# Optimization experiments

Hardware: AMD Instinct MI355X
Metric: run time of the kernel (lower is better)

Reference implementation:

```python
import jax, jax.numpy as jnp
import numpy as np

K = 64        # top-k from init_kwargs
TAU = 1.0     # temperature at step=0: tau_start*(1-0) + tau_end*0


def setup_inputs() -> dict:
    key = jax.random.key(0)
    k1, k2 = jax.random.split(key)
    B, N = 2048, 8192
    logits = jax.random.normal(k1, (B, N), dtype=jnp.float32)
    # gumbels = -log(Exp(1)) == standard Gumbel noise
    gumbel_noise = jax.random.gumbel(k2, (B, N), dtype=jnp.float32)
    return {"logits": logits, "gumbel_noise": gumbel_noise}


def reference(logits, gumbel_noise):
    # training path of GumbelTopK (step=0 -> tau=TAU, hard=True)
    g = (logits + gumbel_noise) / TAU                       # [B, N]
    order = jnp.argsort(-g, axis=-1)                        # descending sort order
    sorted_g = jnp.take_along_axis(g, order, axis=-1)
    cumsum = jnp.cumsum(jax.nn.softmax(sorted_g, axis=-1), axis=-1)
    mask = (cumsum <= K).astype(sorted_g.dtype)             # NB: faithful to source (<= k)
    sorted_y = mask * jax.nn.softmax(sorted_g / TAU, axis=-1)
    # scatter back to original positions == gather by inverse permutation
    inv = jnp.argsort(order, axis=-1)
    y = jnp.take_along_axis(sorted_y, inv, axis=-1)         # [B, N]
    # hard straight-through: one-hot-k of y
    k = min(K, y.shape[-1])
    _, idx = jax.lax.top_k(y, k)                            # [B, k]
    rows = jnp.arange(y.shape[0])[:, None]
    y_hard = jnp.zeros_like(y).at[rows, idx].set(1.0)
    return jax.lax.stop_gradient(y_hard - y) + y
```

## Files before the change

kernel.cpp:

```cpp
#include <hip/hip_runtime.h>

constexpr int N = 8192;
constexpr int K = 64;
constexpr int THREADS = 256;
constexpr int WAVES = THREADS / 64;
constexpr int EPT = N / THREADS;
constexpr int VEC = EPT / 4;
constexpr int SEGCAP = 64;
constexpr int CAP = 1024;

constexpr float FTHRESH = 4.75f;

typedef float f32x4 __attribute__((ext_vector_type(4)));

__device__ __forceinline__ unsigned orderable(float f) {
    unsigned x = __float_as_uint(f);
    return (x & 0x80000000u) ? ~x : (x | 0x80000000u);
}

__device__ __forceinline__ void barrier_nd() {
    asm volatile("s_waitcnt lgkmcnt(0)" ::: "memory");
    __builtin_amdgcn_s_barrier();
    asm volatile("" ::: "memory");
}

__global__ __launch_bounds__(THREADS, 8)
void gumbel_topk_onehot(const float* __restrict__ logits,
                        const float* __restrict__ noise,
                        float* __restrict__ out)
{
    __shared__ __align__(16) unsigned hist[2048];
    __shared__ __align__(16) unsigned cand[CAP];
    __shared__ __align__(16) unsigned seg[WAVES][SEGCAP];
    __shared__ unsigned scnt[WAVES];
    __shared__ unsigned wavesum[WAVES];
    __shared__ unsigned ccount;
    __shared__ unsigned sel_bin, sel_kth, sel_cnt;
    __shared__ unsigned r_val, r_take, r_ceq;

    const int tid  = threadIdx.x;
    const int lane = tid & 63;
    const int wave = tid >> 6;
    const long long row = blockIdx.x;

    const f32x4* l4 = (const f32x4*)(logits + row * (long long)N);
    const f32x4* n4 = (const f32x4*)(noise  + row * (long long)N);
    float s[EPT];
#pragma unroll
    for (int g4 = 0; g4 < VEC; g4 += 2) {
        f32x4 a0 = l4[tid + (g4 + 0) * THREADS];
        f32x4 a1 = l4[tid + (g4 + 1) * THREADS];
        f32x4 b0 = n4[tid + (g4 + 0) * THREADS];
        f32x4 b1 = n4[tid + (g4 + 1) * THREADS];
#pragma unroll
        for (int e = 0; e < 4; ++e) s[4 * g4 + e]     = a0[e] + b0[e];
#pragma unroll
        for (int e = 0; e < 4; ++e) s[4 * g4 + 4 + e] = a1[e] + b1[e];
    }

    const unsigned long long below = (1ull << lane) - 1ull;
    unsigned cw = 0;
#pragma unroll
    for (int e = 0; e < EPT; ++e) {
        const bool p = (s[e] >= FTHRESH);
        const unsigned long long m = __ballot(p);
        if (p) {
            const unsigned pos = cw + (unsigned)__popcll(m & below);
            if (pos < (unsigned)SEGCAP) seg[wave][pos] = __float_as_uint(s[e]);
        }
        cw += (unsigned)__popcll(m);
    }
    if (lane == 0) scnt[wave] = cw;
    barrier_nd();

    const unsigned c0 = scnt[0], c1 = scnt[1], c2 = scnt[2], c3 = scnt[3];
    const unsigned c  = c0 + c1 + c2 + c3;
    const unsigned mx = max(max(c0, c1), max(c2, c3));
    const unsigned cws[WAVES] = {c0, c1, c2, c3};

    float Tf;
    unsigned take_eq, c_eq;
    bool fast;

    if (c >= (unsigned)K && c <= (unsigned)THREADS && mx <= (unsigned)SEGCAP) {
        const bool have = (tid < (int)c);
        unsigned myv = 0u;
        if (have) {
            unsigned d = (unsigned)tid, w2 = 0;
            if (d >= c0) { d -= c0; w2 = 1;
                if (d >= c1) { d -= c1; w2 = 2;
                    if (d >= c2) { d -= c2; w2 = 3; } } }
            myv = seg[w2][d];
        }
        if (tid < (int)((c + 63u) & ~63u)) {
            unsigned g = 0, eq = 0;
#pragma unroll
            for (int w2 = 0; w2 < WAVES; ++w2) {
                const unsigned cn = cws[w2];
                const uint4* s4 = (const uint4*)seg[w2];
                for (unsigned q = 0; q * 4 < cn; ++q) {
                    const uint4 v = s4[q];
                    const unsigned i0 = q * 4;
                    if (i0 + 0 < cn) { g += v.x > myv; eq += v.x == myv; }
                    if (i0 + 1 < cn) { g += v.y > myv; eq += v.y == myv; }
                    if (i0 + 2 < cn) { g += v.z > myv; eq += v.z == myv; }
                    if (i0 + 3 < cn) { g += v.w > myv; eq += v.w == myv; }
                }
            }
            if (have && g < (unsigned)K && g + eq >= (unsigned)K) {
                r_val  = myv;
                r_take = (unsigned)K - g;
                r_ceq  = eq;
            }
        }
        barrier_nd();
        Tf      = __uint_as_float(r_val);
        take_eq = r_take;
        c_eq    = r_ceq;
        fast    = (take_eq == c_eq);
    } else {
        unsigned kth = K;

#define SELECT_BIN(BPT)                                                      \
        {                                                                    \
            unsigned p = 0;                                                  \
            _Pragma("unroll")                                                \
            for (int j = 0; j < (BPT); ++j) p += hist[tid * (BPT) + j];      \
            unsigned sc = p;                                                 \
            _Pragma("unroll")                                                \
            for (int off = 1; off < 64; off <<= 1) {                         \
                unsigned v = __shfl_down(sc, off);                           \
                if (lane + off < 64) sc += v;                                \
            }                                                                \
            if (lane == 0) wavesum[wave] = sc;                               \
            __syncthreads();                                                 \
            unsigned S = sc;                                                 \
            _Pragma("unroll")                                                \
            for (int w = 0; w < WAVES; ++w) if (w > wave) S += wavesum[w];   \
            unsigned Snext = S - p;                                          \
            if (S >= kth && Snext < kth) {                                   \
                unsigned cum = Snext;                                        \
                for (int j = (BPT) - 1; j >= 0; --j) {                       \
                    unsigned b = tid * (BPT) + j;                            \
                    unsigned cc = hist[b];                                   \
                    if (cum + cc >= kth) {                                   \
                        sel_bin = b;                                         \
                        sel_kth = kth - cum;                                 \
                        sel_cnt = cc;                                        \
                        break;                                               \
                    }                                                        \
                    cum += cc;                                               \
                }                                                            \
            }                                                                \
            __syncthreads();                                                 \
        }

        for (int i = tid; i < 512; i += THREADS)
            ((uint4*)hist)[i] = make_uint4(0u, 0u, 0u, 0u);
        if (tid == 0) ccount = 0u;
        __syncthreads();
#pragma unroll
        for (int e = 0; e < EPT; ++e)
            atomicAdd(&hist[orderable(s[e]) >> 21], 1u);
        __syncthreads();
        SELECT_BIN(8)
        const unsigned b1   = sel_bin;
        const unsigned cnt1 = sel_cnt;
        kth = sel_kth;

#pragma unroll
        for (int e = 0; e < EPT; ++e) {
            const unsigned k_e = orderable(s[e]);
            if ((k_e >> 21) == b1) {
                const unsigned pos = atomicAdd(&ccount, 1u);
                if (pos < (unsigned)CAP) cand[pos] = k_e & 0x1FFFFFu;
            }
        }
        __syncthreads();
        const bool use_cand = (cnt1 <= (unsigned)CAP);

        for (int i = tid; i < 512; i += THREADS)
            ((uint4*)hist)[i] = make_uint4(0u, 0u, 0u, 0u);
        __syncthreads();
        if (use_cand) {
            for (int i = tid; i < (int)cnt1; i += THREADS)
                atomicAdd(&hist[cand[i] >> 10], 1u);
        } else {
#pragma unroll
            for (int e = 0; e < EPT; ++e) {
                const unsigned k_e = orderable(s[e]);
                if ((k_e >> 21) == b1)
                    atomicAdd(&hist[(k_e >> 10) & 0x7FFu], 1u);
            }
        }
        __syncthreads();
        SELECT_BIN(8)
        const unsigned b2 = sel_bin;
        kth = sel_kth;
        __syncthreads();

        for (int i = tid; i < 256; i += THREADS)
            ((uint4*)hist)[i] = make_uint4(0u, 0u, 0u, 0u);
        __syncthreads();
        if (use_cand) {
            for (int i = tid; i < (int)cnt1; i += THREADS) {
                const unsigned cv = cand[i];
                if ((cv >> 10) == b2) atomicAdd(&hist[cv & 0x3FFu], 1u);
            }
        } else {
            const unsigned pfx = (b1 << 11) | b2;
#pragma unroll
            for (int e = 0; e < EPT; ++e) {
                const unsigned k_e = orderable(s[e]);
                if ((k_e >> 10) == pfx)
                    atomicAdd(&hist[k_e & 0x3FFu], 1u);
            }
        }
        __syncthreads();
        SELECT_BIN(4)
        const unsigned T_ord = (b1 << 21) | (b2 << 10) | sel_bin;
        const unsigned bits = (T_ord & 0x80000000u) ? (T_ord & 0x7FFFFFFFu)
                                                    : ~T_ord;
        Tf      = __uint_as_float(bits);
        take_eq = sel_kth;
        c_eq    = sel_cnt;
        fast    = (take_eq == c_eq);
#undef SELECT_BIN
    }

    f32x4* orow = (f32x4*)(out + row * (long long)N);
    if (fast) {
#pragma unroll
        for (int i = 0; i < VEC; ++i) {
            f32x4 o;
            o.x = (s[4*i+0] >= Tf) ? 1.0f : 0.0f;
            o.y = (s[4*i+1] >= Tf) ? 1.0f : 0.0f;
            o.z = (s[4*i+2] >= Tf) ? 1.0f : 0.0f;
            o.w = (s[4*i+3] >= Tf) ? 1.0f : 0.0f;
            orow[tid + i * THREADS] = o;
        }
    } else {
#pragma unroll
        for (int i = 0; i < VEC; ++i) {
            f32x4 o;
            o.x = (s[4*i+0] > Tf) ? 1.0f : 0.0f;
            o.y = (s[4*i+1] > Tf) ? 1.0f : 0.0f;
            o.z = (s[4*i+2] > Tf) ? 1.0f : 0.0f;
            o.w = (s[4*i+3] > Tf) ? 1.0f : 0.0f;
            orow[tid + i * THREADS] = o;
        }
        __syncthreads();
        if (tid == 0) {
            const float* lf = logits + row * (long long)N;
            const float* nf = noise  + row * (long long)N;
            float* of = out + row * (long long)N;
            unsigned cc = 0;
            for (int i = 0; i < N; ++i) {
                if (lf[i] + nf[i] == Tf) {
                    of[i] = 1.0f;
                    if (++cc == take_eq) break;
                }
            }
        }
    }
}

extern "C" void kernel_launch(void* const* d_in, const int* in_sizes, int n_in,
                              void* d_out, int out_size, void* d_ws, size_t ws_size,
                              hipStream_t stream) {
    const float* logits = (const float*)d_in[0];
    const float* noise  = (const float*)d_in[1];
    float* out = (float*)d_out;
    const int rows = in_sizes[0] / N;
    gumbel_topk_onehot<<<rows, THREADS, 0, stream>>>(logits, noise, out);
}
```

Baseline: 190.4 us.

## Stream row without register cache, zero-fill output, scatter top-k ones by index

```diff
diff --git a/kernel.cpp b/kernel.cpp
--- a/kernel.cpp
+++ b/kernel.cpp
@@ -4,10 +4,8 @@
 constexpr int K = 64;
 constexpr int THREADS = 256;
 constexpr int WAVES = THREADS / 64;
-constexpr int EPT = N / THREADS;
-constexpr int VEC = EPT / 4;
+constexpr int F4PT = (N / 4) / THREADS;
 constexpr int SEGCAP = 64;
-constexpr int CAP = 1024;
 
 constexpr float FTHRESH = 4.75f;
 
@@ -30,13 +28,13 @@
                         float* __restrict__ out)
 {
     __shared__ __align__(16) unsigned hist[2048];
-    __shared__ __align__(16) unsigned cand[CAP];
-    __shared__ __align__(16) unsigned seg[WAVES][SEGCAP];
+    __shared__ __align__(16) float    segv[WAVES][SEGCAP];
+    __shared__ __align__(16) unsigned segi[WAVES][SEGCAP];
     __shared__ unsigned scnt[WAVES];
     __shared__ unsigned wavesum[WAVES];
-    __shared__ unsigned ccount;
     __shared__ unsigned sel_bin, sel_kth, sel_cnt;
-    __shared__ unsigned r_val, r_take, r_ceq;
+    __shared__ float    sh_T;
+    __shared__ unsigned sh_take, sh_ceq;
 
     const int tid  = threadIdx.x;
     const int lane = tid & 63;
@@ -45,30 +43,39 @@
 
     const f32x4* l4 = (const f32x4*)(logits + row * (long long)N);
     const f32x4* n4 = (const f32x4*)(noise  + row * (long long)N);
-    float s[EPT];
-#pragma unroll
-    for (int g4 = 0; g4 < VEC; g4 += 2) {
-        f32x4 a0 = l4[tid + (g4 + 0) * THREADS];
-        f32x4 a1 = l4[tid + (g4 + 1) * THREADS];
-        f32x4 b0 = n4[tid + (g4 + 0) * THREADS];
-        f32x4 b1 = n4[tid + (g4 + 1) * THREADS];
-#pragma unroll
-        for (int e = 0; e < 4; ++e) s[4 * g4 + e]     = a0[e] + b0[e];
-#pragma unroll
-        for (int e = 0; e < 4; ++e) s[4 * g4 + 4 + e] = a1[e] + b1[e];
-    }
+    f32x4*       o4 = (f32x4*)(out + row * (long long)N);
+    float*     orow = out + row * (long long)N;
 
     const unsigned long long below = (1ull << lane) - 1ull;
+    const f32x4 zero4 = {0.f, 0.f, 0.f, 0.f};
+
     unsigned cw = 0;
 #pragma unroll
-    for (int e = 0; e < EPT; ++e) {
-        const bool p = (s[e] >= FTHRESH);
-        const unsigned long long m = __ballot(p);
-        if (p) {
-            const unsigned pos = cw + (unsigned)__popcll(m & below);
-            if (pos < (unsigned)SEGCAP) seg[wave][pos] = __float_as_uint(s[e]);
-        }
-        cw += (unsigned)__popcll(m);
+    for (int g = 0; g < F4PT; g += 2) {
+        f32x4 a0 = l4[tid + (g + 0) * THREADS];
+        f32x4 a1 = l4[tid + (g + 1) * THREADS];
+        f32x4 b0 = n4[tid + (g + 0) * THREADS];
+        f32x4 b1 = n4[tid + (g + 1) * THREADS];
+        o4[tid + (g + 0) * THREADS] = zero4;
+        o4[tid + (g + 1) * THREADS] = zero4;
+        float sv[8];
+#pragma unroll
+        for (int e = 0; e < 4; ++e) { sv[e] = a0[e] + b0[e]; sv[4 + e] = a1[e] + b1[e]; }
+        const unsigned i0 = 4u * (unsigned)(tid + (g + 0) * THREADS);
+        const unsigned i1 = 4u * (unsigned)(tid + (g + 1) * THREADS);
+#pragma unroll
+        for (int e = 0; e < 8; ++e) {
+            const bool p = (sv[e] >= FTHRESH);
+            const unsigned long long m = __ballot(p);
+            if (p) {
+                const unsigned pos = cw + (unsigned)__popcll(m & below);
+                if (pos < (unsigned)SEGCAP) {
+                    segv[wave][pos] = sv[e];
+                    segi[wave][pos] = (e < 4) ? (i0 + e) : (i1 + e - 4);
+                }
+            }
+            cw += (unsigned)__popcll(m);
+        }
     }
     if (lane == 0) scnt[wave] = cw;
     barrier_nd();
@@ -76,48 +83,59 @@
     const unsigned c0 = scnt[0], c1 = scnt[1], c2 = scnt[2], c3 = scnt[3];
     const unsigned c  = c0 + c1 + c2 + c3;
     const unsigned mx = max(max(c0, c1), max(c2, c3));
-    const unsigned cws[WAVES] = {c0, c1, c2, c3};
-
-    float Tf;
-    unsigned take_eq, c_eq;
-    bool fast;
-
-    if (c >= (unsigned)K && c <= (unsigned)THREADS && mx <= (unsigned)SEGCAP) {
-        const bool have = (tid < (int)c);
-        unsigned myv = 0u;
+
+    if (c >= (unsigned)K && mx <= (unsigned)SEGCAP) {
+        const unsigned cws[WAVES] = {c0, c1, c2, c3};
+        const bool have = ((unsigned)tid < c);
+        float myv = 0.f; unsigned myi = 0;
         if (have) {
             unsigned d = (unsigned)tid, w2 = 0;
             if (d >= c0) { d -= c0; w2 = 1;
                 if (d >= c1) { d -= c1; w2 = 2;
                     if (d >= c2) { d -= c2; w2 = 3; } } }
-            myv = seg[w2][d];
-        }
-        if (tid < (int)((c + 63u) & ~63u)) {
+            myv = segv[w2][d]; myi = segi[w2][d];
+        }
+        if ((unsigned)tid < ((c + 63u) & ~63u)) {
             unsigned g = 0, eq = 0;
 #pragma unroll
             for (int w2 = 0; w2 < WAVES; ++w2) {
                 const unsigned cn = cws[w2];
-                const uint4* s4 = (const uint4*)seg[w2];
+                const f32x4* s4 = (const f32x4*)segv[w2];
                 for (unsigned q = 0; q * 4 < cn; ++q) {
-                    const uint4 v = s4[q];
-                    const unsigned i0 = q * 4;
-                    if (i0 + 0 < cn) { g += v.x > myv; eq += v.x == myv; }
-                    if (i0 + 1 < cn) { g += v.y > myv; eq += v.y == myv; }
-                    if (i0 + 2 < cn) { g += v.z > myv; eq += v.z == myv; }
-                    if (i0 + 3 < cn) { g += v.w > myv; eq += v.w == myv; }
+                    const f32x4 v = s4[q];
+                    const unsigned b = q * 4;
+                    if (b + 0 < cn) { g += v.x > myv; eq += v.x == myv; }
+                    if (b + 1 < cn) { g += v.y > myv; eq += v.y == myv; }
+                    if (b + 2 < cn) { g += v.z > myv; eq += v.z == myv; }
+                    if (b + 3 < cn) { g += v.w > myv; eq += v.w == myv; }
                 }
             }
             if (have && g < (unsigned)K && g + eq >= (unsigned)K) {
-                r_val  = myv;
-                r_take = (unsigned)K - g;
-                r_ceq  = eq;
+                sh_T = myv; sh_take = (unsigned)K - g; sh_ceq = eq;
             }
         }
         barrier_nd();
-        Tf      = __uint_as_float(r_val);
-        take_eq = r_take;
-        c_eq    = r_ceq;
-        fast    = (take_eq == c_eq);
+        const float Tf = sh_T;
+        const unsigned take_eq = sh_take;
+        const bool fast = (take_eq == sh_ceq);
+
+        asm volatile("s_waitcnt vmcnt(0)" ::: "memory");
+        __builtin_amdgcn_s_barrier();
+
+        if (have) {
+            if (myv > Tf || (fast && myv == Tf)) {
+                orow[myi] = 1.0f;
+            } else if (!fast && myv == Tf) {
+                unsigned r = 0;
+#pragma unroll
+                for (int w2 = 0; w2 < WAVES; ++w2) {
+                    const unsigned cn = cws[w2];
+                    for (unsigned q = 0; q < cn; ++q)
+                        r += (segv[w2][q] == Tf) && (segi[w2][q] < myi);
+                }
+                if (r < take_eq) orow[myi] = 1.0f;
+            }
+        }
     } else {
         unsigned kth = K;
 
@@ -157,38 +175,28 @@
 
         for (int i = tid; i < 512; i += THREADS)
             ((uint4*)hist)[i] = make_uint4(0u, 0u, 0u, 0u);
-        if (tid == 0) ccount = 0u;
-        __syncthreads();
-#pragma unroll
-        for (int e = 0; e < EPT; ++e)
-            atomicAdd(&hist[orderable(s[e]) >> 21], 1u);
+        __syncthreads();
+        for (int g = 0; g < F4PT; ++g) {
+            f32x4 a = l4[tid + g * THREADS];
+            f32x4 b = n4[tid + g * THREADS];
+#pragma unroll
+            for (int e = 0; e < 4; ++e)
+                atomicAdd(&hist[orderable(a[e] + b[e]) >> 21], 1u);
+        }
         __syncthreads();
         SELECT_BIN(8)
-        const unsigned b1   = sel_bin;
-        const unsigned cnt1 = sel_cnt;
+        const unsigned b1 = sel_bin;
         kth = sel_kth;
-
-#pragma unroll
-        for (int e = 0; e < EPT; ++e) {
-            const unsigned k_e = orderable(s[e]);
-            if ((k_e >> 21) == b1) {
-                const unsigned pos = atomicAdd(&ccount, 1u);
-                if (pos < (unsigned)CAP) cand[pos] = k_e & 0x1FFFFFu;
-            }
-        }
-        __syncthreads();
-        const bool use_cand = (cnt1 <= (unsigned)CAP);
 
         for (int i = tid; i < 512; i += THREADS)
             ((uint4*)hist)[i] = make_uint4(0u, 0u, 0u, 0u);
         __syncthreads();
-        if (use_cand) {
-            for (int i = tid; i < (int)cnt1; i += THREADS)
-                atomicAdd(&hist[cand[i] >> 10], 1u);
-        } else {
-#pragma unroll
-            for (int e = 0; e < EPT; ++e) {
-                const unsigned k_e = orderable(s[e]);
+        for (int g = 0; g < F4PT; ++g) {
+            f32x4 a = l4[tid + g * THREADS];
+            f32x4 b = n4[tid + g * THREADS];
+#pragma unroll
+            for (int e = 0; e < 4; ++e) {
+                const unsigned k_e = orderable(a[e] + b[e]);
                 if ((k_e >> 21) == b1)
                     atomicAdd(&hist[(k_e >> 10) & 0x7FFu], 1u);
             }
@@ -197,68 +205,50 @@
         SELECT_BIN(8)
         const unsigned b2 = sel_bin;
         kth = sel_kth;
-        __syncthreads();
 
         for (int i = tid; i < 256; i += THREADS)
             ((uint4*)hist)[i] = make_uint4(0u, 0u, 0u, 0u);
         __syncthreads();
-        if (use_cand) {
-            for (int i = tid; i < (int)cnt1; i += THREADS) {
-                const unsigned cv = cand[i];
-                if ((cv >> 10) == b2) atomicAdd(&hist[cv & 0x3FFu], 1u);
-            }
-        } else {
-            const unsigned pfx = (b1 << 11) | b2;
-#pragma unroll
-            for (int e = 0; e < EPT; ++e) {
-                const unsigned k_e = orderable(s[e]);
+        const unsigned pfx = (b1 << 11) | b2;
+        for (int g = 0; g < F4PT; ++g) {
+            f32x4 a = l4[tid + g * THREADS];
+            f32x4 b = n4[tid + g * THREADS];
+#pragma unroll
+            for (int e = 0; e < 4; ++e) {
+                const unsigned k_e = orderable(a[e] + b[e]);
                 if ((k_e >> 10) == pfx)
                     atomicAdd(&hist[k_e & 0x3FFu], 1u);
             }
         }
         __syncthreads();
         SELECT_BIN(4)
-        const unsigned T_ord = (b1 << 21) | (b2 << 10) | sel_bin;
-        const unsigned bits = (T_ord & 0x80000000u) ? (T_ord & 0x7FFFFFFFu)
-                                                    : ~T_ord;
-        Tf      = __uint_as_float(bits);
-        take_eq = sel_kth;
-        c_eq    = sel_cnt;
-        fast    = (take_eq == c_eq);
+        const unsigned T_ord   = (b1 << 21) | (b2 << 10) | sel_bin;
+        const unsigned take_eq = sel_kth;
+        const bool fast = (take_eq == sel_cnt);
 #undef SELECT_BIN
-    }
-
-    f32x4* orow = (f32x4*)(out + row * (long long)N);
-    if (fast) {
-#pragma unroll
-        for (int i = 0; i < VEC; ++i) {
+
+        for (int g = 0; g < F4PT; ++g) {
+            f32x4 a = l4[tid + g * THREADS];
+            f32x4 b = n4[tid + g * THREADS];
             f32x4 o;
-            o.x = (s[4*i+0] >= Tf) ? 1.0f : 0.0f;
-            o.y = (s[4*i+1] >= Tf) ? 1.0f : 0.0f;
-            o.z = (s[4*i+2] >= Tf) ? 1.0f : 0.0f;
-            o.w = (s[4*i+3] >= Tf) ? 1.0f : 0.0f;
-            orow[tid + i * THREADS] = o;
-        }
-    } else {
-#pragma unroll
-        for (int i = 0; i < VEC; ++i) {
-            f32x4 o;
-            o.x = (s[4*i+0] > Tf) ? 1.0f : 0.0f;
-            o.y = (s[4*i+1] > Tf) ? 1.0f : 0.0f;
-            o.z = (s[4*i+2] > Tf) ? 1.0f : 0.0f;
-            o.w = (s[4*i+3] > Tf) ? 1.0f : 0.0f;
-            orow[tid + i * THREADS] = o;
-        }
-        __syncthreads();
-        if (tid == 0) {
-            const float* lf = logits + row * (long long)N;
-            const float* nf = noise  + row * (long long)N;
-            float* of = out + row * (long long)N;
-            unsigned cc = 0;
-            for (int i = 0; i < N; ++i) {
-                if (lf[i] + nf[i] == Tf) {
-                    of[i] = 1.0f;
-                    if (++cc == take_eq) break;
+#pragma unroll
+            for (int e = 0; e < 4; ++e) {
+                const unsigned k_e = orderable(a[e] + b[e]);
+                o[e] = (k_e > T_ord || (fast && k_e == T_ord)) ? 1.0f : 0.0f;
+            }
+            o4[tid + g * THREADS] = o;
+        }
+        if (!fast) {
+            __syncthreads();
+            if (tid == 0) {
+                const float* lf = logits + row * (long long)N;
+                const float* nf = noise  + row * (long long)N;
+                unsigned cc = 0;
+                for (int i = 0; i < N; ++i) {
+                    if (orderable(lf[i] + nf[i]) == T_ord) {
+                        orow[i] = 1.0f;
+                        if (++cc == take_eq) break;
+                    }
                 }
             }
         }
```

Result: faster. 185.6 us (-2.5%).
